# Performance work log

Hardware: AMD Instinct MI355X
Metric: run time of the kernel (lower is better)

## Reference

```python
import jax, jax.numpy as jnp
import numpy as np
import math

D_INNER = 512
D_STATE = 16
DT_RANK = 32
B_SZ = 2
L_SEQ = 4096


def setup_inputs() -> dict:
    key = jax.random.key(0)
    ks = jax.random.split(key, 6)
    x = jax.random.normal(ks[0], (B_SZ, L_SEQ, D_INNER), dtype=jnp.float32)
    # parameters (match torch init semantics closely enough for a numeric baseline)
    A = jnp.arange(1, D_STATE + 1, dtype=jnp.float32)
    A_log = jnp.broadcast_to(jnp.log(A)[None, :], (D_INNER, D_STATE)).copy()
    D_param = jnp.ones((D_INNER,), dtype=jnp.float32)
    # x_proj: Linear(d_inner -> dt_rank + 2*d_state), no bias
    W_xproj = jax.random.normal(ks[1], (DT_RANK + 2 * D_STATE, D_INNER), dtype=jnp.float32) / np.sqrt(D_INNER)
    # dt_proj: Linear(dt_rank -> d_inner) with special bias init
    W_dt = jax.random.normal(ks[2], (D_INNER, DT_RANK), dtype=jnp.float32) / np.sqrt(DT_RANK)
    dt_init = jnp.exp(jax.random.uniform(ks[3], (D_INNER,)) * (math.log(0.1) - math.log(0.001)) + math.log(0.001))
    b_dt = jnp.log(jnp.exp(dt_init) - 1.0)
    alpha = jnp.asarray(0.6, dtype=jnp.float32)
    beta_logit = jnp.asarray(math.log(0.99 / (1.0 - 0.99 + 1e-08)), dtype=jnp.float32)
    return {"x": x, "A_log": A_log, "D_param": D_param, "W_xproj": W_xproj,
            "W_dt": W_dt, "b_dt": b_dt, "alpha": alpha, "beta_logit": beta_logit}


def _momentum_ssm(x, A_log, D_param, W_xproj, W_dt, b_dt, alpha, beta_logit):
    # x: (B, L, D)
    proj = jnp.einsum('bld,pd->blp', x, W_xproj)            # (B, L, r+2N)
    dt_in = proj[..., :DT_RANK]
    Bp = proj[..., DT_RANK:DT_RANK + D_STATE]                # (B, L, N)
    Cp = proj[..., DT_RANK + D_STATE:]                       # (B, L, N)
    dt = jax.nn.softplus(jnp.einsum('blr,dr->bld', dt_in, W_dt) + b_dt)  # (B, L, D)
    A = -jnp.exp(A_log)                                      # (D, N)
    A_bar = jnp.exp(dt[..., None] * A[None, None])           # (B, L, D, N)
    # fused B_bar * x_t: dt * Bp * x
    inp = dt[..., None] * Bp[:, :, None, :] * x[..., None]   # (B, L, D, N)
    beta = jax.nn.sigmoid(beta_logit)

    # scan over time; carry (h, v): (B, D, N)
    h0 = jnp.zeros((x.shape[0], D_INNER, D_STATE), dtype=x.dtype)
    v0 = jnp.zeros_like(h0)

    def step(carry, ts):
        h, v = carry
        a_t, inp_t, c_t = ts                                 # (B,D,N), (B,D,N), (B,N)
        v = beta * v + alpha * inp_t
        h = a_t * h + v
        y = jnp.einsum('bdn,bn->bd', h, c_t)
        return (h, v), y

    xs = (jnp.moveaxis(A_bar, 1, 0), jnp.moveaxis(inp, 1, 0), jnp.moveaxis(Cp, 1, 0))
    _, ys = jax.lax.scan(step, (h0, v0), xs)                 # ys: (L, B, D)
    y = jnp.moveaxis(ys, 0, 1)                               # (B, L, D)
    return y + D_param * x


def reference(x, A_log, D_param, W_xproj, W_dt, b_dt, alpha, beta_logit):
    return _momentum_ssm(x, A_log, D_param, W_xproj, W_dt, b_dt, alpha, beta_logit)
```

## Files before the change

kernel.cpp:

```cpp
#include <hip/hip_runtime.h>


#define D_IN 512
#define D_ST 16
#define DTR  32
#define BSZ  2
#define LSEQ 4096
#define PDIM 64
#define NCH  256
#define LCH  (LSEQ / NCH)
#define LOG2E 1.44269504f
#define LN2   0.69314718f

typedef __attribute__((ext_vector_type(8))) short short8;
typedef __attribute__((ext_vector_type(4))) float f32x4;
typedef _Float16 f16;
typedef __attribute__((ext_vector_type(8))) _Float16 f16x8;

__device__ inline float fast_exp2(float x) { return __builtin_amdgcn_exp2f(x); }
__device__ inline float fast_log2(float x) { return __builtin_amdgcn_logf(x); }

__device__ inline unsigned short bf16_rne(float f) {
  unsigned b = __float_as_uint(f);
  return (unsigned short)((b + 0x7fffu + ((b >> 16) & 1u)) >> 16);
}

__device__ inline void cvt8(const float4 u, const float4 v, short8& hi, short8& lo) {
  float f[8] = {u.x, u.y, u.z, u.w, v.x, v.y, v.z, v.w};
#pragma unroll
  for (int i = 0; i < 8; ++i) {
    unsigned short h = bf16_rne(f[i]);
    hi[i] = (short)h;
    float r = f[i] - __uint_as_float((unsigned)h << 16);
    lo[i] = (short)bf16_rne(r);
  }
}

__device__ inline void st16h(f16* p, const float* s) {
  f16 t[16];
#pragma unroll
  for (int i = 0; i < 16; ++i) t[i] = (f16)s[i];
  *(f16x8*)p = *(f16x8*)&t[0];
  *(f16x8*)(p + 8) = *(f16x8*)&t[8];
}
__device__ inline void ld16h(const f16* p, float* d) {
  f16x8 a = *(const f16x8*)p;
  f16x8 b = *(const f16x8*)(p + 8);
#pragma unroll
  for (int i = 0; i < 8; ++i) { d[i] = (float)a[i]; d[8 + i] = (float)b[i]; }
}

#define PWCHK(val, n)                                                        \
  pw = pw && (fabsf((val) - (float)((n) + 1) * a0) <=                        \
              2e-5f * fabsf((float)((n) + 1) * a0));

__device__ inline bool detectA2(const float* __restrict__ A_log, int d, float& a0) {
  const float4* ap = (const float4*)(A_log + (size_t)d * D_ST);
  float4 r0 = ap[0], r1 = ap[1], r2 = ap[2], r3 = ap[3];
  float4 e0 = make_float4(-__expf(r0.x) * LOG2E, -__expf(r0.y) * LOG2E,
                          -__expf(r0.z) * LOG2E, -__expf(r0.w) * LOG2E);
  float4 e1 = make_float4(-__expf(r1.x) * LOG2E, -__expf(r1.y) * LOG2E,
                          -__expf(r1.z) * LOG2E, -__expf(r1.w) * LOG2E);
  float4 e2 = make_float4(-__expf(r2.x) * LOG2E, -__expf(r2.y) * LOG2E,
                          -__expf(r2.z) * LOG2E, -__expf(r2.w) * LOG2E);
  float4 e3 = make_float4(-__expf(r3.x) * LOG2E, -__expf(r3.y) * LOG2E,
                          -__expf(r3.z) * LOG2E, -__expf(r3.w) * LOG2E);
  a0 = e0.x;
  bool pw = true;
  PWCHK(e0.y, 1) PWCHK(e0.z, 2) PWCHK(e0.w, 3)
  PWCHK(e1.x, 4) PWCHK(e1.y, 5) PWCHK(e1.z, 6) PWCHK(e1.w, 7)
  PWCHK(e2.x, 8) PWCHK(e2.y, 9) PWCHK(e2.z, 10) PWCHK(e2.w, 11)
  PWCHK(e3.x, 12) PWCHK(e3.y, 13) PWCHK(e3.z, 14) PWCHK(e3.w, 15)
  return pw;
}

#define MM3(ACC, AH, AL, BH, BL)                                        \
  ACC = __builtin_amdgcn_mfma_f32_16x16x32_bf16(AL, BH, ACC, 0, 0, 0);  \
  ACC = __builtin_amdgcn_mfma_f32_16x16x32_bf16(AH, BL, ACC, 0, 0, 0);  \
  ACC = __builtin_amdgcn_mfma_f32_16x16x32_bf16(AH, BH, ACC, 0, 0, 0);

#define LOADBF(P, S)                                          \
  {                                                           \
    const int kb = (S) * 32;                                  \
    float4 a0 = *(const float4*)(wr + kb);                    \
    float4 b0 = *(const float4*)(wr + kb + 4);                \
    float4 a1 = *(const float4*)(wr + 8192 + kb);             \
    float4 b1 = *(const float4*)(wr + 8192 + kb + 4);         \
    float4 a2 = *(const float4*)(wr + 16384 + kb);            \
    float4 b2 = *(const float4*)(wr + 16384 + kb + 4);        \
    float4 a3 = *(const float4*)(wr + 24576 + kb);            \
    float4 b3 = *(const float4*)(wr + 24576 + kb + 4);        \
    cvt8(a0, b0, P##h0, P##l0);                               \
    cvt8(a1, b1, P##h1, P##l1);                               \
    cvt8(a2, b2, P##h2, P##l2);                               \
    cvt8(a3, b3, P##h3, P##l3);                               \
  }

#define LOADA(Aa, Ab, S)                              \
  {                                                   \
    const int ka = (S) * 32;                          \
    Aa = *(const float4*)(xr + ka);                   \
    Ab = *(const float4*)(xr + ka + 4);               \
  }

#define COMPSTEP(Aa, Ab, P)                           \
  {                                                   \
    short8 ahi, alo;                                  \
    cvt8(Aa, Ab, ahi, alo);                           \
    MM3(acc0, ahi, alo, P##h0, P##l0);                \
    MM3(acc1, ahi, alo, P##h1, P##l1);                \
    MM3(acc2, ahi, alo, P##h2, P##l2);                \
    MM3(acc3, ahi, alo, P##h3, P##l3);                \
  }

__global__ __launch_bounds__(256) void k_proj(const float* __restrict__ x,
                                              const float* __restrict__ W,
                                              float* __restrict__ proj) {
  __shared__ float Pacc[4][16][64];
  const int row0 = blockIdx.x * 16;
  const int l = threadIdx.x & 63;
  const int wq = threadIdx.x >> 6;
  const int m = l & 15;
  const int ko = (l >> 4) * 8 + wq * 128;
  const float* xr = x + (size_t)(row0 + m) * D_IN + ko;
  const float* wr = W + (size_t)m * D_IN + ko;

  f32x4 acc0 = {0.f, 0.f, 0.f, 0.f}, acc1 = acc0, acc2 = acc0, acc3 = acc0;
  float4 A0a, A0b, A1a, A1b, A2a, A2b, A3a, A3b;
  short8 Xh0, Xh1, Xh2, Xh3, Xl0, Xl1, Xl2, Xl3;
  short8 Yh0, Yh1, Yh2, Yh3, Yl0, Yl1, Yl2, Yl3;
  LOADA(A0a, A0b, 0); LOADA(A1a, A1b, 1); LOADA(A2a, A2b, 2); LOADA(A3a, A3b, 3);
  LOADBF(X, 0); LOADBF(Y, 1);

  COMPSTEP(A0a, A0b, X); LOADBF(X, 2);
  COMPSTEP(A1a, A1b, Y); LOADBF(Y, 3);
  COMPSTEP(A2a, A2b, X);
  COMPSTEP(A3a, A3b, Y);

  const int r0 = (l >> 4) * 4;
#pragma unroll
  for (int r = 0; r < 4; ++r) {
    Pacc[wq][r0 + r][m] = acc0[r];
    Pacc[wq][r0 + r][16 + m] = acc1[r];
    Pacc[wq][r0 + r][32 + m] = acc2[r];
    Pacc[wq][r0 + r][48 + m] = acc3[r];
  }
  __syncthreads();

  const int orow = threadIdx.x >> 4;
  const int ocol = (threadIdx.x & 15) * 4;
  float4 s0 = *(const float4*)&Pacc[0][orow][ocol];
  float4 s1 = *(const float4*)&Pacc[1][orow][ocol];
  float4 s2 = *(const float4*)&Pacc[2][orow][ocol];
  float4 s3 = *(const float4*)&Pacc[3][orow][ocol];
  float4 o = make_float4((s0.x + s1.x) + (s2.x + s3.x), (s0.y + s1.y) + (s2.y + s3.y),
                         (s0.z + s1.z) + (s2.z + s3.z), (s0.w + s1.w) + (s2.w + s3.w));
  *(float4*)(proj + (size_t)(row0 + orow) * PDIM + ocol) = o;
}

#define S1_LOOP                                                              \
  _Pragma("unroll")                                                          \
  for (int j = 0; j < LCH; ++j) {                                            \
    const float4* pj = (const float4*)(pb + j * PDIM);                       \
    float4 pp[8];                                                            \
    _Pragma("unroll")                                                        \
    for (int k = 0; k < 8; ++k) pp[k] = pj[k];                               \
    float c0 = bb, c1 = 0.f, c2 = 0.f, c3 = 0.f;                             \
    _Pragma("unroll")                                                        \
    for (int k = 0; k < 8; ++k) {                                            \
      c0 = fmaf(pp[k].x, w4[k].x, c0);                                       \
      c1 = fmaf(pp[k].y, w4[k].y, c1);                                       \
      c2 = fmaf(pp[k].z, w4[k].z, c2);                                       \
      c3 = fmaf(pp[k].w, w4[k].w, c3);                                       \
    }                                                                        \
    const float acc = (c0 + c1) + (c2 + c3);                                 \
    const float ee = fast_exp2(acc * LOG2E);                                 \
    const float dtc = (acc > 20.f) ? acc : LN2 * fast_log2(1.f + ee);        \
    dp[(size_t)j * D_IN] = (f16)dtc;                                         \
    sd += dtc;                                                               \
    bpow *= beta;                                                            \
    const float u = alpha * dtc * xs[j];                                     \
    float4 bq[4];                                                            \
    _Pragma("unroll")                                                        \
    for (int k = 0; k < 4; ++k) bq[k] = pj[8 + k];                           \
    const float* Bf = (const float*)bq;                                      \
    AR_INIT;                                                                 \
    _Pragma("unroll")                                                        \
    for (int n = 0; n < 16; ++n) {                                           \
      AR_STEP;                                                               \
      v[n] = fmaf(beta, v[n], u * Bf[n]);                                    \
      h[n] = fmaf(ar, h[n], v[n]);                                           \
      cv[n] = fmaf(ar, cv[n], bpow);                                         \
    }                                                                        \
  }

__global__ __launch_bounds__(256) void k_scan1(const float* __restrict__ x,
                                               const float* __restrict__ proj,
                                               const float* __restrict__ A_log,
                                               const float* __restrict__ W_dt,
                                               const float* __restrict__ b_dt,
                                               const float* __restrict__ alpha_p,
                                               const float* __restrict__ beta_p,
                                               f16* __restrict__ hh,
                                               f16* __restrict__ vh,
                                               f16* __restrict__ cvv,
                                               float* __restrict__ sdt,
                                               f16* __restrict__ dth) {
  const int c = blockIdx.x, b = blockIdx.z;
  const int d = blockIdx.y * 256 + threadIdx.x;
  const int t0 = c * LCH;
  const float* pb = proj + ((size_t)b * LSEQ + t0) * PDIM;

  float xs[LCH];
  {
    const float* xp = x + ((size_t)b * LSEQ + t0) * D_IN + d;
#pragma unroll
    for (int j = 0; j < LCH; ++j) xs[j] = xp[(size_t)j * D_IN];
  }
  float4 w4[8];
  {
    const float4* wp = (const float4*)(W_dt + (size_t)d * DTR);
#pragma unroll
    for (int i = 0; i < 8; ++i) w4[i] = wp[i];
  }
  const float bb = b_dt[d];
  const float alpha = alpha_p[0];
  const float beta = 1.f / (1.f + __expf(-beta_p[0]));
  float a0;
  const bool pw = detectA2(A_log, d, a0);

  f16* dp = dth + ((size_t)b * LSEQ + t0) * D_IN + d;
  float h[16] = {}, v[16] = {}, cv[16] = {};
  float bpow = 1.f, sd = 0.f;

  if (pw) {
#define AR_INIT const float r = fast_exp2(dtc * a0); float ar = 1.f
#define AR_STEP ar *= r
    S1_LOOP
#undef AR_INIT
#undef AR_STEP
  } else {
    volatile const float* av = A_log + (size_t)d * D_ST;
#define AR_INIT float ar
#define AR_STEP ar = fast_exp2(dtc * (-__expf(av[n]) * LOG2E))
    S1_LOOP
#undef AR_INIT
#undef AR_STEP
  }

  const size_t base = ((size_t)(b * NCH + c) * D_IN + d) * D_ST;
  st16h(hh + base, h);
  st16h(vh + base, v);
  st16h(cvv + base, cv);
  sdt[(size_t)(b * NCH + c) * D_IN + d] = sd;
}

__global__ __launch_bounds__(64) void k_fix(f16* __restrict__ hh,
                                            f16* __restrict__ vh,
                                            const f16* __restrict__ cvv,
                                            const float* __restrict__ sdt,
                                            const float* __restrict__ A_log,
                                            const float* __restrict__ beta_p) {
  const int g = blockIdx.x * 64 + threadIdx.x;
  const int b = g >> 13;
  const int dn = g & 8191;
  const float beta = 1.f / (1.f + __expf(-beta_p[0]));
  const float A2 = -__expf(A_log[dn]) * LOG2E;
  float bL = beta;
#pragma unroll
  for (int i = 0; i < 4; ++i) bL *= bL;

  const size_t cs = (size_t)D_IN * D_ST;
  const size_t base = (size_t)b * NCH * cs + dn;
  const size_t sbase = (size_t)b * NCH * D_IN + (dn >> 4);

  float hg[16], vg[16], cg[16], sg[16];
#pragma unroll
  for (int i = 0; i < 16; ++i) {
    hg[i] = (float)hh[base + i * cs];
    vg[i] = (float)vh[base + i * cs];
    cg[i] = (float)cvv[base + i * cs];
    sg[i] = sdt[sbase + i * D_IN];
  }
  float H = 0.f, V = 0.f;
  for (int c0 = 0; c0 < NCH; c0 += 16) {
    const int cp = (c0 + 16) & (NCH - 1);
    float hn[16], vn[16], cn[16], sn[16];
#pragma unroll
    for (int i = 0; i < 16; ++i) {
      hn[i] = (float)hh[base + (size_t)(cp + i) * cs];
      vn[i] = (float)vh[base + (size_t)(cp + i) * cs];
      cn[i] = (float)cvv[base + (size_t)(cp + i) * cs];
      sn[i] = sdt[sbase + (size_t)(cp + i) * D_IN];
    }
#pragma unroll
    for (int i = 0; i < 16; ++i) {
      hh[base + (size_t)(c0 + i) * cs] = (f16)H;
      vh[base + (size_t)(c0 + i) * cs] = (f16)V;
      const float Pa = fast_exp2(sg[i] * A2);
      const float Hn = fmaf(Pa, H, fmaf(cg[i], V, hg[i]));
      V = fmaf(bL, V, vg[i]);
      H = Hn;
    }
#pragma unroll
    for (int i = 0; i < 16; ++i) { hg[i] = hn[i]; vg[i] = vn[i]; cg[i] = cn[i]; sg[i] = sn[i]; }
  }
}

#define S2_LOOP                                                              \
  _Pragma("unroll")                                                          \
  for (int j = 0; j < LCH; ++j) {                                            \
    const float4* pj = (const float4*)(pb + j * PDIM);                       \
    float4 bq[8];                                                            \
    _Pragma("unroll")                                                        \
    for (int k = 0; k < 8; ++k) bq[k] = pj[8 + k];                           \
    const float* Bf = (const float*)bq;                                      \
    const float dtc = dtv[j], xv = xs[j];                                    \
    const float u = alpha * dtc * xv;                                        \
    float y0 = 0.f, y1 = 0.f, y2 = 0.f, y3 = 0.f;                            \
    AR_INIT;                                                                 \
    _Pragma("unroll")                                                        \
    for (int n = 0; n < 16; ++n) {                                           \
      AR_STEP;                                                               \
      v[n] = fmaf(beta, v[n], u * Bf[n]);                                    \
      h[n] = fmaf(ar, h[n], v[n]);                                           \
      float hc = h[n] * Bf[16 + n];                                          \
      if ((n & 3) == 0) y0 += hc;                                            \
      else if ((n & 3) == 1) y1 += hc;                                       \
      else if ((n & 3) == 2) y2 += hc;                                       \
      else y3 += hc;                                                         \
    }                                                                        \
    op[(size_t)j * D_IN] = (y0 + y1) + (y2 + y3) + Dv * xv;                  \
  }

__global__ __launch_bounds__(256) void k_scan2(const float* __restrict__ x,
                                               const f16* __restrict__ dth,
                                               const float* __restrict__ proj,
                                               const float* __restrict__ A_log,
                                               const float* __restrict__ D_param,
                                               const float* __restrict__ alpha_p,
                                               const float* __restrict__ beta_p,
                                               const f16* __restrict__ hh,
                                               const f16* __restrict__ vh,
                                               float* __restrict__ out) {
  const int c = blockIdx.x, b = blockIdx.z;
  const int d = blockIdx.y * 256 + threadIdx.x;
  const int t0 = c * LCH;
  const float* pb = proj + ((size_t)b * LSEQ + t0) * PDIM;

  float xs[LCH], dtv[LCH];
  {
    const float* xp = x + ((size_t)b * LSEQ + t0) * D_IN + d;
    const f16* dp = dth + ((size_t)b * LSEQ + t0) * D_IN + d;
#pragma unroll
    for (int j = 0; j < LCH; ++j) xs[j] = xp[(size_t)j * D_IN];
#pragma unroll
    for (int j = 0; j < LCH; ++j) dtv[j] = (float)dp[(size_t)j * D_IN];
  }
  const float alpha = alpha_p[0];
  const float beta = 1.f / (1.f + __expf(-beta_p[0]));
  const float Dv = D_param[d];
  float a0;
  const bool pw = detectA2(A_log, d, a0);
  const size_t ibase = ((size_t)(b * NCH + c) * D_IN + d) * D_ST;
  float h[16], v[16];
  ld16h(hh + ibase, h);
  ld16h(vh + ibase, v);

  float* op = out + ((size_t)b * LSEQ + t0) * D_IN + d;
  if (pw) {
#define AR_INIT const float r = fast_exp2(dtc * a0); float ar = 1.f
#define AR_STEP ar *= r
    S2_LOOP
#undef AR_INIT
#undef AR_STEP
  } else {
    volatile const float* av = A_log + (size_t)d * D_ST;
#define AR_INIT float ar
#define AR_STEP ar = fast_exp2(dtc * (-__expf(av[n]) * LOG2E))
    S2_LOOP
#undef AR_INIT
#undef AR_STEP
  }
}

extern "C" void kernel_launch(void* const* d_in, const int* in_sizes, int n_in,
                              void* d_out, int out_size, void* d_ws, size_t ws_size,
                              hipStream_t stream) {
  const float* x = (const float*)d_in[0];
  const float* A_log = (const float*)d_in[1];
  const float* D_param = (const float*)d_in[2];
  const float* W_xproj = (const float*)d_in[3];
  const float* W_dt = (const float*)d_in[4];
  const float* b_dt = (const float*)d_in[5];
  const float* alpha = (const float*)d_in[6];
  const float* beta_logit = (const float*)d_in[7];
  float* out = (float*)d_out;

  const size_t NST = (size_t)BSZ * NCH * D_IN * D_ST;
  float* ws = (float*)d_ws;
  float* proj = ws;
  float* sdt = proj + (size_t)BSZ * LSEQ * PDIM;
  f16* hh = (f16*)(sdt + (size_t)BSZ * NCH * D_IN);
  f16* vh = hh + NST;
  f16* cvv = vh + NST;
  f16* dth = cvv + NST;

  k_proj<<<dim3(BSZ * LSEQ / 16), dim3(256), 0, stream>>>(x, W_xproj, proj);
  k_scan1<<<dim3(NCH, D_IN / 256, BSZ), dim3(256), 0, stream>>>(
      x, proj, A_log, W_dt, b_dt, alpha, beta_logit, hh, vh, cvv, sdt, dth);
  k_fix<<<dim3(BSZ * D_IN * D_ST / 64), dim3(64), 0, stream>>>(hh, vh, cvv, sdt, A_log,
                                                               beta_logit);
  k_scan2<<<dim3(NCH, D_IN / 256, BSZ), dim3(256), 0, stream>>>(
      x, dth, proj, A_log, D_param, alpha, beta_logit, hh, vh, out);
}
```

Measured before the change: 166.3 us.

## Parallelize chunk-carry fixup with 16-lane shuffle scan over chunk spans

The fixup kernel previously walked all 256 chunks sequentially per (b,d,n) state with one thread each. Now 16 lanes each own 16 chunks: each computes a local affine-composition summary (P, q, h, v, w) for the momentum recurrence, then a Hillis-Steele shuffle scan combines the summaries across lanes, and each lane replays its 16 chunks to write carry-in states. This shortens the serial dependency chain and raises thread count, at the cost of extra arithmetic, shuffles and less coalesced memory access across chunks.

```diff
diff --git a/kernel.cpp b/kernel.cpp
--- a/kernel.cpp
+++ b/kernel.cpp
@@ -255,13 +255,16 @@
   sdt[(size_t)(b * NCH + c) * D_IN + d] = sd;
 }
 
-__global__ __launch_bounds__(64) void k_fix(f16* __restrict__ hh,
-                                            f16* __restrict__ vh,
-                                            const f16* __restrict__ cvv,
-                                            const float* __restrict__ sdt,
-                                            const float* __restrict__ A_log,
-                                            const float* __restrict__ beta_p) {
-  const int g = blockIdx.x * 64 + threadIdx.x;
+__global__ __launch_bounds__(256) void k_fix(f16* __restrict__ hh,
+                                             f16* __restrict__ vh,
+                                             const f16* __restrict__ cvv,
+                                             const float* __restrict__ sdt,
+                                             const float* __restrict__ A_log,
+                                             const float* __restrict__ beta_p) {
+  const int lane = threadIdx.x & 63;
+  const int wv = threadIdx.x >> 6;
+  const int span = lane & 15;
+  const int g = blockIdx.x * 16 + wv * 4 + (lane >> 4);
   const int b = g >> 13;
   const int dn = g & 8191;
   const float beta = 1.f / (1.f + __expf(-beta_p[0]));
@@ -271,39 +274,58 @@
   for (int i = 0; i < 4; ++i) bL *= bL;
 
   const size_t cs = (size_t)D_IN * D_ST;
+  const int c0 = span * 16;
   const size_t base = (size_t)b * NCH * cs + dn;
   const size_t sbase = (size_t)b * NCH * D_IN + (dn >> 4);
 
-  float hg[16], vg[16], cg[16], sg[16];
+  float hc[16], vc[16], cvc[16], Pa[16];
 #pragma unroll
   for (int i = 0; i < 16; ++i) {
-    hg[i] = (float)hh[base + i * cs];
-    vg[i] = (float)vh[base + i * cs];
-    cg[i] = (float)cvv[base + i * cs];
-    sg[i] = sdt[sbase + i * D_IN];
-  }
-  float H = 0.f, V = 0.f;
-  for (int c0 = 0; c0 < NCH; c0 += 16) {
-    const int cp = (c0 + 16) & (NCH - 1);
-    float hn[16], vn[16], cn[16], sn[16];
-#pragma unroll
-    for (int i = 0; i < 16; ++i) {
-      hn[i] = (float)hh[base + (size_t)(cp + i) * cs];
-      vn[i] = (float)vh[base + (size_t)(cp + i) * cs];
-      cn[i] = (float)cvv[base + (size_t)(cp + i) * cs];
-      sn[i] = sdt[sbase + (size_t)(cp + i) * D_IN];
+    const int c = c0 + i;
+    hc[i] = (float)hh[base + (size_t)c * cs];
+    vc[i] = (float)vh[base + (size_t)c * cs];
+    cvc[i] = (float)cvv[base + (size_t)c * cs];
+    Pa[i] = fast_exp2(sdt[sbase + (size_t)c * D_IN] * A2);
+  }
+  float SP = 1.f, Sq = 0.f, Sh = 0.f, Sv = 0.f, Sw = 1.f;
+#pragma unroll
+  for (int i = 0; i < 16; ++i) {
+    Sq = fmaf(Pa[i], Sq, cvc[i] * Sw);
+    Sh = fmaf(Pa[i], Sh, fmaf(cvc[i], Sv, hc[i]));
+    SP = Pa[i] * SP;
+    Sv = fmaf(bL, Sv, vc[i]);
+    Sw = bL * Sw;
+  }
+
+#pragma unroll
+  for (int s = 1; s < 16; s <<= 1) {
+    float AP = __shfl_up(SP, s, 16);
+    float Aq = __shfl_up(Sq, s, 16);
+    float Ah = __shfl_up(Sh, s, 16);
+    float Av = __shfl_up(Sv, s, 16);
+    float Aw = __shfl_up(Sw, s, 16);
+    if (span >= s) {
+      const float nP = SP * AP;
+      const float nq = fmaf(SP, Aq, Sq * Aw);
+      const float nh = fmaf(SP, Ah, fmaf(Sq, Av, Sh));
+      const float nv = fmaf(Sw, Av, Sv);
+      const float nw = Sw * Aw;
+      SP = nP; Sq = nq; Sh = nh; Sv = nv; Sw = nw;
     }
-#pragma unroll
-    for (int i = 0; i < 16; ++i) {
-      hh[base + (size_t)(c0 + i) * cs] = (f16)H;
-      vh[base + (size_t)(c0 + i) * cs] = (f16)V;
-      const float Pa = fast_exp2(sg[i] * A2);
-      const float Hn = fmaf(Pa, H, fmaf(cg[i], V, hg[i]));
-      V = fmaf(bL, V, vg[i]);
-      H = Hn;
-    }
-#pragma unroll
-    for (int i = 0; i < 16; ++i) { hg[i] = hn[i]; vg[i] = vn[i]; cg[i] = cn[i]; sg[i] = sn[i]; }
+  }
+
+  float H = __shfl_up(Sh, 1, 16);
+  float V = __shfl_up(Sv, 1, 16);
+  if (span == 0) { H = 0.f; V = 0.f; }
+
+#pragma unroll
+  for (int i = 0; i < 16; ++i) {
+    const int c = c0 + i;
+    hh[base + (size_t)c * cs] = (f16)H;
+    vh[base + (size_t)c * cs] = (f16)V;
+    const float Hn = fmaf(Pa[i], H, fmaf(cvc[i], V, hc[i]));
+    V = fmaf(bL, V, vc[i]);
+    H = Hn;
   }
 }
 
@@ -409,8 +431,8 @@
   k_proj<<<dim3(BSZ * LSEQ / 16), dim3(256), 0, stream>>>(x, W_xproj, proj);
   k_scan1<<<dim3(NCH, D_IN / 256, BSZ), dim3(256), 0, stream>>>(
       x, proj, A_log, W_dt, b_dt, alpha, beta_logit, hh, vh, cvv, sdt, dth);
-  k_fix<<<dim3(BSZ * D_IN * D_ST / 64), dim3(64), 0, stream>>>(hh, vh, cvv, sdt, A_log,
-                                                               beta_logit);
+  k_fix<<<dim3(BSZ * D_IN * D_ST / 16), dim3(256), 0, stream>>>(hh, vh, cvv, sdt, A_log,
+                                                                beta_logit);
   k_scan2<<<dim3(NCH, D_IN / 256, BSZ), dim3(256), 0, stream>>>(
       x, dth, proj, A_log, D_param, alpha, beta_logit, hh, vh, out);
 }
```

After: 192.0 us. 1.15x slower.
